# Optimization experiments

Hardware: AMD Instinct MI355X
Metric: run time of the kernel (lower is better)

## Reference

```python
import jax, jax.numpy as jnp
import numpy as np

# Scale constants (production tokenizer-style)
P = 1_048_576   # total flat byte-params (sum of token lengths over vocab)
E = 8_388_608   # occurrence edges: (token-instance, byte-within-token) pairs
T = 4_194_304   # text length in bytes
N = 2_097_152   # number of token instances (valid_tokens)
INIT_STD = 0.02


def setup_inputs() -> dict:
    key = jax.random.key(0)
    k1, k2, k3, k4 = jax.random.split(key, 4)
    flat_params = jax.random.normal(k1, (P,), dtype=jnp.float32) * INIT_STD
    # occ_param_idx[e] = offset[token_id_e] + byte_idx_e  (index into flat param vector)
    occ_param_idx = jax.random.randint(k2, (E,), 0, P, dtype=jnp.int32)
    # occ_byte_pos[e] = start_pos_e + byte_idx_e  (absolute byte position in text)
    occ_byte_pos = jax.random.randint(k3, (E,), 0, T, dtype=jnp.int32)
    # occ_token_idx[e] = which token instance this byte occurrence belongs to
    occ_token_idx = jax.random.randint(k4, (E,), 0, N, dtype=jnp.int32)
    return {
        "flat_params": flat_params,
        "occ_param_idx": occ_param_idx,
        "occ_byte_pos": occ_byte_pos,
        "occ_token_idx": occ_token_idx,
        "text_len": T,
        "num_tokens": N,
    }


def reference(flat_params, occ_param_idx, occ_byte_pos, occ_token_idx, text_len, num_tokens):
    # 1) gather per-occurrence byte params
    vals = flat_params[occ_param_idx]                                      # [E]
    # 2) scatter-add into byte positions: sum and count per byte
    byte_sum = jax.ops.segment_sum(vals, occ_byte_pos, num_segments=text_len)            # [T]
    byte_cnt = jax.ops.segment_sum(jnp.ones_like(vals), occ_byte_pos, num_segments=text_len)  # [T]
    # 3) mean per byte (0 where no token covers the byte, as in the torch code)
    byte_w = jnp.where(byte_cnt > 0, byte_sum / jnp.maximum(byte_cnt, 1.0), 0.0)          # [T]
    # 4) each token's position = sum of byte weights over its span
    positions = jax.ops.segment_sum(byte_w[occ_byte_pos], occ_token_idx, num_segments=num_tokens)  # [N]
    return positions
```

## Files before the change

### kernel.cpp

```cpp
#include <hip/hip_runtime.h>


typedef unsigned long long u64;
typedef unsigned int uint;
typedef int  vi4  __attribute__((ext_vector_type(4)));
typedef unsigned long long uv2 __attribute__((ext_vector_type(2)));

constexpr int NB   = 512;
constexpr int PPB  = 8192;
constexpr int NB2  = 256;
constexpr int TOKB = 8192;
constexpr int CAP  = 17408;
constexpr int CAP2 = 34816;

constexpr float V_SCALE = 2097152.0f;
constexpr float V_INV   = 1.0f / 2097152.0f;
constexpr float W_SCALE = 524288.0f;
constexpr float W_INV   = 1.0f / 524288.0f;

__device__ __forceinline__ void wave_scan512(const uint* hist, uint* lbase,
                                             int t) {
    if (t < 64) {
        uint h[8];
        uint run = 0;
        #pragma unroll
        for (int j = 0; j < 8; ++j) { h[j] = run; run += hist[t * 8 + j]; }
        uint tot = run, inc = tot;
        #pragma unroll
        for (int d = 1; d < 64; d <<= 1) {
            uint up = __shfl_up(inc, d, 64);
            if (t >= d) inc += up;
        }
        uint excl = inc - tot;
        #pragma unroll
        for (int j = 0; j < 8; ++j) lbase[t * 8 + j] = excl + h[j];
        if (t == 63) lbase[512] = inc;
    }
}

__device__ __forceinline__ void wave_scan256(const uint* hist, uint* lbase,
                                             int t) {
    if (t < 64) {
        uint h[4];
        uint run = 0;
        #pragma unroll
        for (int j = 0; j < 4; ++j) { h[j] = run; run += hist[t * 4 + j]; }
        uint tot = run, inc = tot;
        #pragma unroll
        for (int d = 1; d < 64; d <<= 1) {
            uint up = __shfl_up(inc, d, 64);
            if (t >= d) inc += up;
        }
        uint excl = inc - tot;
        #pragma unroll
        for (int j = 0; j < 4; ++j) lbase[t * 4 + j] = excl + h[j];
        if (t == 63) lbase[256] = inc;
    }
}

constexpr int A_THREADS = 1024;
constexpr int A_EPT     = 8;
constexpr int A_CHUNK   = A_THREADS * A_EPT;
constexpr int A_CPB     = 2;

__global__ __launch_bounds__(A_THREADS, 8) void phaseA(
    const int* __restrict__ pidx, const int* __restrict__ bpos,
    const int* __restrict__ tidx, u64* __restrict__ recs,
    uint* __restrict__ gcur, int E)
{
    __shared__ u64 stage[A_CHUNK];
    __shared__ uint hist[NB], lcur[NB], gbase[NB], lbase[NB + 1];
    int t = threadIdx.x;

    int c = blockIdx.x * A_CPB;
    int be0 = c * A_CHUNK + t * A_EPT;
    bool vec = (be0 + A_EPT) <= E;

    vi4 b0, b1, p0, p1, k0, k1;
    if (vec) {
        b0 = __builtin_nontemporal_load((const vi4*)(bpos + be0));
        b1 = __builtin_nontemporal_load((const vi4*)(bpos + be0 + 4));
        p0 = __builtin_nontemporal_load((const vi4*)(pidx + be0));
        p1 = __builtin_nontemporal_load((const vi4*)(pidx + be0 + 4));
        k0 = __builtin_nontemporal_load((const vi4*)(tidx + be0));
        k1 = __builtin_nontemporal_load((const vi4*)(tidx + be0 + 4));
    }

    for (int cc = 0; cc < A_CPB; ++cc, ++c) {
        if (t < NB) { hist[t] = 0u; lcur[t] = 0u; }
        __syncthreads();

        int be = c * A_CHUNK + t * A_EPT;
        if (vec) {
            atomicAdd(&hist[((uint)b0.x) >> 13], 1u);
            atomicAdd(&hist[((uint)b0.y) >> 13], 1u);
            atomicAdd(&hist[((uint)b0.z) >> 13], 1u);
            atomicAdd(&hist[((uint)b0.w) >> 13], 1u);
            atomicAdd(&hist[((uint)b1.x) >> 13], 1u);
            atomicAdd(&hist[((uint)b1.y) >> 13], 1u);
            atomicAdd(&hist[((uint)b1.z) >> 13], 1u);
            atomicAdd(&hist[((uint)b1.w) >> 13], 1u);
        } else {
            for (int j = 0; j < A_EPT; ++j) {
                int e = be + j;
                if (e < E) atomicAdd(&hist[((uint)bpos[e]) >> 13], 1u);
            }
        }
        __syncthreads();

        wave_scan512(hist, lbase, t);
        if (t >= 512) gbase[t - 512] = atomicAdd(&gcur[t - 512], hist[t - 512]);
        __syncthreads();

        auto emit = [&](int p, int tk, int pi) {
            uint b = ((uint)p) >> 13;
            u64 rec = (u64)(uint)(p & (PPB - 1))
                    | ((u64)(uint)tk << 13)
                    | ((u64)(uint)pi << 34)
                    | ((u64)b << 55);
            uint off = lbase[b] + atomicAdd(&lcur[b], 1u);
            stage[off] = rec;
        };
        if (vec) {
            emit(b0.x, k0.x, p0.x); emit(b0.y, k0.y, p0.y);
            emit(b0.z, k0.z, p0.z); emit(b0.w, k0.w, p0.w);
            emit(b1.x, k1.x, p1.x); emit(b1.y, k1.y, p1.y);
            emit(b1.z, k1.z, p1.z); emit(b1.w, k1.w, p1.w);
        } else {
            for (int j = 0; j < A_EPT; ++j) {
                int e = be + j;
                if (e < E) emit(bpos[e], tidx[e], pidx[e]);
            }
        }

        bool nvec = false;
        if (cc + 1 < A_CPB) {
            int nbe = (c + 1) * A_CHUNK + t * A_EPT;
            nvec = (nbe + A_EPT) <= E;
            if (nvec) {
                b0 = __builtin_nontemporal_load((const vi4*)(bpos + nbe));
                b1 = __builtin_nontemporal_load((const vi4*)(bpos + nbe + 4));
                p0 = __builtin_nontemporal_load((const vi4*)(pidx + nbe));
                p1 = __builtin_nontemporal_load((const vi4*)(pidx + nbe + 4));
                k0 = __builtin_nontemporal_load((const vi4*)(tidx + nbe));
                k1 = __builtin_nontemporal_load((const vi4*)(tidx + nbe + 4));
            }
        }
        __syncthreads();

        uint total = lbase[NB];
        for (uint i = t; i < total; i += A_THREADS) {
            u64 rc = stage[i];
            int b = (int)(rc >> 55);
            uint dst = gbase[b] + (i - lbase[b]);
            if (dst < (uint)CAP)
                recs[(size_t)b * CAP + dst] = rc;
        }
        vec = nvec;
    }
}

constexpr int C_THREADS = 1024;
constexpr int C_CHUNK   = 8192;
constexpr int C_MAXCH   = (CAP + C_CHUNK - 1) / C_CHUNK;

__global__ __launch_bounds__(C_THREADS, 8) void phaseC(
    const float* __restrict__ fp,
    const u64* __restrict__ recs, const uint* __restrict__ gcur,
    uint* __restrict__ rec2, uint* __restrict__ gcur2)
{
    __shared__ uint acc[PPB];
    __shared__ uint stage2[C_CHUNK];
    __shared__ uint histc[C_MAXCH][NB2];
    __shared__ uint lcur[NB2], gb[NB2], lbase[NB2 + 1];
    int t = threadIdx.x;
    int b = blockIdx.x;
    for (int i = t; i < PPB; i += C_THREADS) acc[i] = 0u;
    for (int i = t; i < C_MAXCH * NB2; i += C_THREADS) (&histc[0][0])[i] = 0u;
    if (t < NB2) lcur[t] = 0u;
    __syncthreads();

    uint n = min(gcur[b], (uint)CAP);
    const u64* r = recs + (size_t)b * CAP;

    auto process = [&](u64 rc, uint ch) {
        uint pos = (uint)rc & (PPB - 1);
        uint pi  = (uint)(rc >> 34) & 0x1FFFFFu;
        int  fx  = (int)rintf(fp[pi] * V_SCALE);
        atomicAdd(&acc[pos], (uint)((1 << 26) + fx));
        atomicAdd(&histc[ch][(uint)(rc >> 26) & 0xFFu], 1u);
    };
    uint np = n >> 1;
    for (uint i = t; i < np; i += C_THREADS) {
        uv2 rr = __builtin_nontemporal_load(((const uv2*)r) + i);
        uint ch = (2u * i) / C_CHUNK;
        process(rr.x, ch); process(rr.y, ch);
    }
    for (uint i = 2u * np + t; i < n; i += C_THREADS)
        process(__builtin_nontemporal_load(r + i), i / C_CHUNK);
    __syncthreads();

    if (t >= 512 && t < 512 + NB2) {
        int tb = t - 512;
        uint tot = histc[0][tb];
        #pragma unroll
        for (int c = 1; c < C_MAXCH; ++c) tot += histc[c][tb];
        gb[tb] = atomicAdd(&gcur2[tb], tot);
    }

    uint ch = 0;
    for (uint c0 = 0; c0 < n; c0 += C_CHUNK, ++ch) {
        uint m = min((uint)C_CHUNK, n - c0);
        wave_scan256(histc[ch], lbase, t);
        __syncthreads();
        for (uint i = t; i < m; i += C_THREADS) {
            u64 rc = __builtin_nontemporal_load(r + c0 + i);
            uint pos = (uint)rc & (PPB - 1);
            uint tok = (uint)(rc >> 13) & 0x1FFFFFu;
            uint a = acc[pos];
            uint c = (a + (1u << 25)) >> 26;
            int s = (int)(a - (c << 26));
            float w = (float)s * V_INV / (float)c;
            int wfx = (int)rintf(w * W_SCALE);
            uint tb = tok >> 13;
            uint off = lbase[tb] + atomicAdd(&lcur[tb], 1u);
            stage2[off] = (tok & (TOKB - 1)) | ((uint)wfx << 13);
        }
        __syncthreads();
        int w = t >> 6, lane = t & 63;
        for (int tb = w; tb < NB2; tb += 16) {
            uint base = lbase[tb];
            uint len  = lbase[tb + 1] - base;
            uint g    = gb[tb];
            for (uint j = lane; j < len; j += 64) {
                uint dst = g + j;
                if (dst < (uint)CAP2)
                    rec2[(size_t)tb * CAP2 + dst] = stage2[base + j];
            }
        }
        __syncthreads();
        if (t < NB2) { gb[t] += histc[ch][t]; lcur[t] = 0u; }
        __syncthreads();
    }
}

constexpr int D_THREADS = 1024;

__global__ __launch_bounds__(D_THREADS) void phaseD(
    const uint* __restrict__ rec2, const uint* __restrict__ gcur2,
    float* __restrict__ out, int N)
{
    __shared__ int facc[TOKB];
    int t = threadIdx.x;
    int b = blockIdx.x;
    for (int i = t; i < TOKB; i += D_THREADS) facc[i] = 0;
    __syncthreads();
    uint n = min(gcur2[b], (uint)CAP2);
    const uint* r = rec2 + (size_t)b * CAP2;
    uint nq = n >> 2;
    for (uint i = t; i < nq; i += D_THREADS) {
        uint4 q = ((const uint4*)r)[i];
        atomicAdd(&facc[q.x & (TOKB - 1)], ((int)q.x) >> 13);
        atomicAdd(&facc[q.y & (TOKB - 1)], ((int)q.y) >> 13);
        atomicAdd(&facc[q.z & (TOKB - 1)], ((int)q.z) >> 13);
        atomicAdd(&facc[q.w & (TOKB - 1)], ((int)q.w) >> 13);
    }
    for (uint i = 4u * nq + t; i < n; i += D_THREADS) {
        uint rc = r[i];
        atomicAdd(&facc[rc & (TOKB - 1)], ((int)rc) >> 13);
    }
    __syncthreads();
    int base = b * TOKB;
    for (int i = t; i < TOKB; i += D_THREADS) {
        int idx = base + i;
        if (idx < N)
            __builtin_nontemporal_store((float)facc[i] * W_INV, &out[idx]);
    }
}

__global__ void fb_scatter(const float* __restrict__ fp,
                           const int* __restrict__ pidx,
                           const int* __restrict__ bpos,
                           u64* __restrict__ bacc, int E) {
    int e = blockIdx.x * blockDim.x + threadIdx.x;
    if (e < E) {
        float v = fp[pidx[e]];
        long long fx = (long long)rintf(v * 4294967296.0f);
        atomicAdd(&bacc[bpos[e]], (1ULL << 39) + (u64)fx);
    }
}

__global__ void fb_tokens(const u64* __restrict__ bacc,
                          const int* __restrict__ bpos,
                          const int* __restrict__ tidx,
                          float* __restrict__ out, int E) {
    int e = blockIdx.x * blockDim.x + threadIdx.x;
    if (e < E) {
        u64 v = bacc[bpos[e]];
        long long cnt = (long long)((v + (1ULL << 38)) >> 39);
        long long s   = (long long)(v - ((u64)cnt << 39));
        atomicAdd(&out[tidx[e]], (float)s * (1.0f / 4294967296.0f) / (float)cnt);
    }
}

extern "C" void kernel_launch(void* const* d_in, const int* in_sizes, int n_in,
                              void* d_out, int out_size, void* d_ws, size_t ws_size,
                              hipStream_t stream) {
    const float* flat_params   = (const float*)d_in[0];
    const int*   occ_param_idx = (const int*)d_in[1];
    const int*   occ_byte_pos  = (const int*)d_in[2];
    const int*   occ_token_idx = (const int*)d_in[3];

    const int P = in_sizes[0];
    const int E = in_sizes[1];
    const int N = out_size;

    const size_t REC_BYTES  = (size_t)NB  * CAP  * 8;
    const size_t REC2_BYTES = (size_t)NB2 * CAP2 * 4;
    const size_t NEED = 4096 + REC_BYTES + REC2_BYTES;

    if (ws_size >= NEED && N <= NB2 * TOKB && P <= (1 << 21)) {
        uint* gcur  = (uint*)d_ws;
        uint* gcur2 = (uint*)((char*)d_ws + 2048);
        u64* recs = (u64*)((char*)d_ws + 4096);
        uint* rec2 = (uint*)((char*)d_ws + 4096 + REC_BYTES);

        (void)hipMemsetAsync(d_ws, 0, 4096, stream);

        int nchunks = (E + A_CHUNK - 1) / A_CHUNK;
        int gridA = (nchunks + A_CPB - 1) / A_CPB;
        phaseA<<<gridA, A_THREADS, 0, stream>>>(occ_param_idx, occ_byte_pos,
                                                occ_token_idx, recs, gcur, E);
        phaseC<<<NB, C_THREADS, 0, stream>>>(flat_params, recs, gcur,
                                             rec2, gcur2);
        phaseD<<<NB2, D_THREADS, 0, stream>>>(rec2, gcur2, (float*)d_out, N);
    } else {
        u64* bacc = (u64*)d_ws;
        (void)hipMemsetAsync(bacc, 0, (size_t)4194304 * 8, stream);
        (void)hipMemsetAsync(d_out, 0, (size_t)N * sizeof(float), stream);
        int gridE = (E + 255) / 256;
        fb_scatter<<<gridE, 256, 0, stream>>>(flat_params, occ_param_idx,
                                              occ_byte_pos, bacc, E);
        fb_tokens<<<gridE, 256, 0, stream>>>(bacc, occ_byte_pos,
                                             occ_token_idx, (float*)d_out, E);
    }
}
```

Baseline: 248.5 us.

## Use 512 token buckets of 4096 and batch gathers/loads for memory-level parallelism

Doubles the number of second-pass token buckets (512 buckets of 4096 tokens, smaller per-bucket capacity), so phase D runs twice as many blocks with a smaller shared accumulator. The packed record now carries a 20-bit weight field instead of 19. Phase C's main loops are manually unrolled to issue several record loads and parameter gathers before the shared-memory atomics, and phase D's loop is unrolled the same way, to raise memory-level parallelism. Risks include reduced weight precision headroom, overflow of the smaller per-bucket capacity under skew, and more scan and histogram work per chunk.

After: 254.6 us. 2.4% more time.

```diff
diff --git a/kernel.cpp b/kernel.cpp
--- a/kernel.cpp
+++ b/kernel.cpp
@@ -8,10 +8,10 @@
 
 constexpr int NB   = 512;
 constexpr int PPB  = 8192;
-constexpr int NB2  = 256;
-constexpr int TOKB = 8192;
+constexpr int NB2  = 512;
+constexpr int TOKB = 4096;
 constexpr int CAP  = 17408;
-constexpr int CAP2 = 34816;
+constexpr int CAP2 = 17408;
 
 constexpr float V_SCALE = 2097152.0f;
 constexpr float V_INV   = 1.0f / 2097152.0f;
@@ -35,26 +35,6 @@
         #pragma unroll
         for (int j = 0; j < 8; ++j) lbase[t * 8 + j] = excl + h[j];
         if (t == 63) lbase[512] = inc;
-    }
-}
-
-__device__ __forceinline__ void wave_scan256(const uint* hist, uint* lbase,
-                                             int t) {
-    if (t < 64) {
-        uint h[4];
-        uint run = 0;
-        #pragma unroll
-        for (int j = 0; j < 4; ++j) { h[j] = run; run += hist[t * 4 + j]; }
-        uint tot = run, inc = tot;
-        #pragma unroll
-        for (int d = 1; d < 64; d <<= 1) {
-            uint up = __shfl_up(inc, d, 64);
-            if (t >= d) inc += up;
-        }
-        uint excl = inc - tot;
-        #pragma unroll
-        for (int j = 0; j < 4; ++j) lbase[t * 4 + j] = excl + h[j];
-        if (t == 63) lbase[256] = inc;
     }
 }
 
@@ -183,24 +163,50 @@
     uint n = min(gcur[b], (uint)CAP);
     const u64* r = recs + (size_t)b * CAP;
 
-    auto process = [&](u64 rc, uint ch) {
-        uint pos = (uint)rc & (PPB - 1);
-        uint pi  = (uint)(rc >> 34) & 0x1FFFFFu;
-        int  fx  = (int)rintf(fp[pi] * V_SCALE);
-        atomicAdd(&acc[pos], (uint)((1 << 26) + fx));
-        atomicAdd(&histc[ch][(uint)(rc >> 26) & 0xFFu], 1u);
+    auto upd = [&](u64 rc, float v, uint ch) {
+        int fx = (int)rintf(v * V_SCALE);
+        atomicAdd(&acc[(uint)rc & (PPB - 1)], (uint)((1 << 26) + fx));
+        atomicAdd(&histc[ch][(uint)(rc >> 25) & 0x1FFu], 1u);
     };
     uint np = n >> 1;
-    for (uint i = t; i < np; i += C_THREADS) {
-        uv2 rr = __builtin_nontemporal_load(((const uv2*)r) + i);
-        uint ch = (2u * i) / C_CHUNK;
-        process(rr.x, ch); process(rr.y, ch);
-    }
-    for (uint i = 2u * np + t; i < n; i += C_THREADS)
-        process(__builtin_nontemporal_load(r + i), i / C_CHUNK);
+    const uv2* pr = (const uv2*)r;
+    uint i = t;
+    for (; i + 3u * C_THREADS < np; i += 4u * C_THREADS) {
+        uv2 x0 = __builtin_nontemporal_load(pr + i);
+        uv2 x1 = __builtin_nontemporal_load(pr + i + C_THREADS);
+        uv2 x2 = __builtin_nontemporal_load(pr + i + 2u * C_THREADS);
+        uv2 x3 = __builtin_nontemporal_load(pr + i + 3u * C_THREADS);
+        float v0 = fp[(uint)(x0.x >> 34) & 0x1FFFFFu];
+        float v1 = fp[(uint)(x0.y >> 34) & 0x1FFFFFu];
+        float v2 = fp[(uint)(x1.x >> 34) & 0x1FFFFFu];
+        float v3 = fp[(uint)(x1.y >> 34) & 0x1FFFFFu];
+        float v4 = fp[(uint)(x2.x >> 34) & 0x1FFFFFu];
+        float v5 = fp[(uint)(x2.y >> 34) & 0x1FFFFFu];
+        float v6 = fp[(uint)(x3.x >> 34) & 0x1FFFFFu];
+        float v7 = fp[(uint)(x3.y >> 34) & 0x1FFFFFu];
+        uint c0 = i >> 12;
+        uint c1 = (i + C_THREADS) >> 12;
+        uint c2 = (i + 2u * C_THREADS) >> 12;
+        uint c3 = (i + 3u * C_THREADS) >> 12;
+        upd(x0.x, v0, c0); upd(x0.y, v1, c0);
+        upd(x1.x, v2, c1); upd(x1.y, v3, c1);
+        upd(x2.x, v4, c2); upd(x2.y, v5, c2);
+        upd(x3.x, v6, c3); upd(x3.y, v7, c3);
+    }
+    for (; i < np; i += C_THREADS) {
+        uv2 x = __builtin_nontemporal_load(pr + i);
+        uint ch = i >> 12;
+        float va = fp[(uint)(x.x >> 34) & 0x1FFFFFu];
+        float vb = fp[(uint)(x.y >> 34) & 0x1FFFFFu];
+        upd(x.x, va, ch); upd(x.y, vb, ch);
+    }
+    if ((n & 1u) && t == 0) {
+        u64 rc = __builtin_nontemporal_load(r + n - 1);
+        upd(rc, fp[(uint)(rc >> 34) & 0x1FFFFFu], (n - 1) / C_CHUNK);
+    }
     __syncthreads();
 
-    if (t >= 512 && t < 512 + NB2) {
+    if (t >= 512) {
         int tb = t - 512;
         uint tot = histc[0][tb];
         #pragma unroll
@@ -208,23 +214,44 @@
         gb[tb] = atomicAdd(&gcur2[tb], tot);
     }
 
+    auto emit = [&](u64 rc, uint a) {
+        uint tok = (uint)(rc >> 13) & 0x1FFFFFu;
+        uint c = (a + (1u << 25)) >> 26;
+        int s = (int)(a - (c << 26));
+        float w = (float)s * V_INV / (float)c;
+        int wfx = (int)rintf(w * W_SCALE);
+        uint tb = tok >> 12;
+        uint off = lbase[tb] + atomicAdd(&lcur[tb], 1u);
+        stage2[off] = (tok & (TOKB - 1)) | ((uint)wfx << 12);
+    };
     uint ch = 0;
     for (uint c0 = 0; c0 < n; c0 += C_CHUNK, ++ch) {
         uint m = min((uint)C_CHUNK, n - c0);
-        wave_scan256(histc[ch], lbase, t);
-        __syncthreads();
-        for (uint i = t; i < m; i += C_THREADS) {
-            u64 rc = __builtin_nontemporal_load(r + c0 + i);
-            uint pos = (uint)rc & (PPB - 1);
-            uint tok = (uint)(rc >> 13) & 0x1FFFFFu;
-            uint a = acc[pos];
-            uint c = (a + (1u << 25)) >> 26;
-            int s = (int)(a - (c << 26));
-            float w = (float)s * V_INV / (float)c;
-            int wfx = (int)rintf(w * W_SCALE);
-            uint tb = tok >> 13;
-            uint off = lbase[tb] + atomicAdd(&lcur[tb], 1u);
-            stage2[off] = (tok & (TOKB - 1)) | ((uint)wfx << 13);
+        wave_scan512(histc[ch], lbase, t);
+        __syncthreads();
+
+        uint mp = m >> 1;
+        const uv2* pc = (const uv2*)(r + c0);
+        uint j = t;
+        for (; j + C_THREADS < mp; j += 2u * C_THREADS) {
+            uv2 x0 = __builtin_nontemporal_load(pc + j);
+            uv2 x1 = __builtin_nontemporal_load(pc + j + C_THREADS);
+            uint a0 = acc[(uint)x0.x & (PPB - 1)];
+            uint a1 = acc[(uint)x0.y & (PPB - 1)];
+            uint a2 = acc[(uint)x1.x & (PPB - 1)];
+            uint a3 = acc[(uint)x1.y & (PPB - 1)];
+            emit(x0.x, a0); emit(x0.y, a1);
+            emit(x1.x, a2); emit(x1.y, a3);
+        }
+        for (; j < mp; j += C_THREADS) {
+            uv2 x = __builtin_nontemporal_load(pc + j);
+            uint a0 = acc[(uint)x.x & (PPB - 1)];
+            uint a1 = acc[(uint)x.y & (PPB - 1)];
+            emit(x.x, a0); emit(x.y, a1);
+        }
+        if ((m & 1u) && t == 0) {
+            u64 rc = __builtin_nontemporal_load(r + c0 + m - 1);
+            emit(rc, acc[(uint)rc & (PPB - 1)]);
         }
         __syncthreads();
         int w = t >> 6, lane = t & 63;
@@ -232,10 +259,10 @@
             uint base = lbase[tb];
             uint len  = lbase[tb + 1] - base;
             uint g    = gb[tb];
-            for (uint j = lane; j < len; j += 64) {
-                uint dst = g + j;
+            for (uint q = lane; q < len; q += 64) {
+                uint dst = g + q;
                 if (dst < (uint)CAP2)
-                    rec2[(size_t)tb * CAP2 + dst] = stage2[base + j];
+                    rec2[(size_t)tb * CAP2 + dst] = stage2[base + q];
             }
         }
         __syncthreads();
@@ -257,24 +284,37 @@
     __syncthreads();
     uint n = min(gcur2[b], (uint)CAP2);
     const uint* r = rec2 + (size_t)b * CAP2;
-    uint nq = n >> 2;
-    for (uint i = t; i < nq; i += D_THREADS) {
+    uint n4 = n >> 2;
+    uint i = t;
+    for (; i + D_THREADS < n4; i += 2u * D_THREADS) {
+        uint4 q0 = ((const uint4*)r)[i];
+        uint4 q1 = ((const uint4*)r)[i + D_THREADS];
+        atomicAdd(&facc[q0.x & (TOKB - 1)], ((int)q0.x) >> 12);
+        atomicAdd(&facc[q0.y & (TOKB - 1)], ((int)q0.y) >> 12);
+        atomicAdd(&facc[q0.z & (TOKB - 1)], ((int)q0.z) >> 12);
+        atomicAdd(&facc[q0.w & (TOKB - 1)], ((int)q0.w) >> 12);
+        atomicAdd(&facc[q1.x & (TOKB - 1)], ((int)q1.x) >> 12);
+        atomicAdd(&facc[q1.y & (TOKB - 1)], ((int)q1.y) >> 12);
+        atomicAdd(&facc[q1.z & (TOKB - 1)], ((int)q1.z) >> 12);
+        atomicAdd(&facc[q1.w & (TOKB - 1)], ((int)q1.w) >> 12);
+    }
+    for (; i < n4; i += D_THREADS) {
         uint4 q = ((const uint4*)r)[i];
-        atomicAdd(&facc[q.x & (TOKB - 1)], ((int)q.x) >> 13);
-        atomicAdd(&facc[q.y & (TOKB - 1)], ((int)q.y) >> 13);
-        atomicAdd(&facc[q.z & (TOKB - 1)], ((int)q.z) >> 13);
-        atomicAdd(&facc[q.w & (TOKB - 1)], ((int)q.w) >> 13);
-    }
-    for (uint i = 4u * nq + t; i < n; i += D_THREADS) {
-        uint rc = r[i];
-        atomicAdd(&facc[rc & (TOKB - 1)], ((int)rc) >> 13);
+        atomicAdd(&facc[q.x & (TOKB - 1)], ((int)q.x) >> 12);
+        atomicAdd(&facc[q.y & (TOKB - 1)], ((int)q.y) >> 12);
+        atomicAdd(&facc[q.z & (TOKB - 1)], ((int)q.z) >> 12);
+        atomicAdd(&facc[q.w & (TOKB - 1)], ((int)q.w) >> 12);
+    }
+    for (uint k = (n4 << 2) + t; k < n; k += D_THREADS) {
+        uint rc = r[k];
+        atomicAdd(&facc[rc & (TOKB - 1)], ((int)rc) >> 12);
     }
     __syncthreads();
     int base = b * TOKB;
-    for (int i = t; i < TOKB; i += D_THREADS) {
-        int idx = base + i;
+    for (int i2 = t; i2 < TOKB; i2 += D_THREADS) {
+        int idx = base + i2;
         if (idx < N)
-            __builtin_nontemporal_store((float)facc[i] * W_INV, &out[idx]);
+            __builtin_nontemporal_store((float)facc[i2] * W_INV, &out[idx]);
     }
 }
 
```
